# Performance work log

Measured on AMD Instinct MI355X. Metric: run time of the kernel, lower is better.

The kernel has to match this reference:

```python
import jax, jax.numpy as jnp
import numpy as np

SHORT = 2000
CUTVALS = [0, 2000, 12000, 40000, 100000]  # [0] + cutoffs + [n_classes]
OSZ = [10000, 28000, 60000]
HSZ = [384, 192, 96]
IN_F = 768
LN_EPS = 1e-5


def setup_inputs() -> dict:
    key = jax.random.key(0)
    ks = jax.random.split(key, 16)
    B, L = 256, 20
    inp = {
        "x": jax.random.normal(ks[0], (B, IN_F), jnp.float32),
        "head_W": jax.random.normal(ks[1], (SHORT + 3, IN_F), jnp.float32) / np.sqrt(IN_F),
        "target": jax.random.randint(ks[2], (B, L), 0, CUTVALS[-1], jnp.int64)
        if jax.config.jax_enable_x64 else jax.random.randint(ks[2], (B, L), 0, CUTVALS[-1], jnp.int32),
    }
    for i in range(3):
        inp[f"w1_{i}"] = jax.random.normal(ks[3 + 4 * i], (HSZ[i], IN_F), jnp.float32) / np.sqrt(IN_F)
        inp[f"g{i}"] = jnp.ones((HSZ[i],), jnp.float32)
        inp[f"b{i}"] = jnp.zeros((HSZ[i],), jnp.float32)
        inp[f"w2_{i}"] = jax.random.normal(ks[4 + 4 * i], (OSZ[i], HSZ[i]), jnp.float32) / np.sqrt(HSZ[i])
    return inp


def _bce_with_logits(logits, y):
    # matches torch BCEWithLogitsLoss(reduction='none')
    return jnp.maximum(logits, 0.0) - logits * y + jnp.log1p(jnp.exp(-jnp.abs(logits)))


def reference(x, head_W, w1_0, g0, b0, w2_0, w1_1, g1, b1, w2_1, w1_2, g2, b2, w2_2, target):
    W1, G, Bp, W2 = [w1_0, w1_1, w1_2], [g0, g1, g2], [b0, b1, b2], [w2_0, w2_1, w2_2]
    B = x.shape[0]
    rows = jnp.arange(B)[:, None]
    dt = x.dtype

    head_logits = x @ head_W.T  # [B, SHORT + n_clusters]

    # shortlist multi-hot (rows with no shortlist label stay all-zero, as in torch)
    m0 = target < SHORT
    onehot_short = jnp.zeros((B, SHORT), dt).at[rows, jnp.clip(target, 0, SHORT - 1)].max(m0.astype(dt))

    total_cluster = jnp.zeros((B,), dt)
    actives = []
    for i in range(3):
        low, high = CUTVALS[i + 1], CUTVALS[i + 2]
        osz = high - low
        m = (target >= low) & (target < high)  # [B, L]
        active = m.any(axis=1).astype(dt)      # [B]
        actives.append(active)
        # multi-hot targets for this cluster
        y = jnp.zeros((B, osz), dt).at[rows, jnp.clip(target - low, 0, osz - 1)].max(m.astype(dt))
        # tail projection: Linear -> LayerNorm -> ReLU -> Linear
        h = x @ W1[i].T
        mu = h.mean(-1, keepdims=True)
        var = ((h - mu) ** 2).mean(-1, keepdims=True)
        h = jax.nn.relu((h - mu) * jax.lax.rsqrt(var + LN_EPS) * G[i] + Bp[i])
        # p = sigmoid(cluster-root logit) * sigmoid(tail logits)
        root = jax.nn.sigmoid(head_logits[:, SHORT + i])[:, None]  # [B,1]
        p = root * jax.nn.sigmoid(h @ W2[i].T)                     # [B, osz]
        # torch BCELoss clamps log at -100
        bce = -(y * jnp.maximum(jnp.log(p), -100.0) + (1.0 - y) * jnp.maximum(jnp.log1p(-p), -100.0))
        total_cluster = total_cluster + active * bce.sum(axis=1)

    cluster_onehot = jnp.stack(actives, axis=1)  # [B, 3]
    head_y = jnp.concatenate([onehot_short, cluster_onehot], axis=1)
    head_loss = _bce_with_logits(head_logits, head_y)  # [B, SHORT+3]
    mult = (cluster_onehot == 0).astype(dt)
    head_loss = jnp.concatenate([head_loss[:, :SHORT], head_loss[:, SHORT:] * mult], axis=1)
    head_loss = head_loss.sum(axis=1)

    csz = jnp.asarray(OSZ, dt)
    num_loss = (mult + cluster_onehot * csz).sum(axis=1) + SHORT
    return ((head_loss + total_cluster) / num_loss).mean()
```

## Files before the change

### kernel.cpp

```cpp
#include <hip/hip_runtime.h>
#include <hip/hip_bf16.h>

#define INF 768
#define NSHORT 2000
#define NHEAD 2003

typedef __attribute__((ext_vector_type(8))) short  s16x8;
typedef __attribute__((ext_vector_type(4))) float  f32x4;
typedef __attribute__((ext_vector_type(8))) float  f32x8;

__device__ __forceinline__ float sigf(float z) { return 1.f / (1.f + __expf(-z)); }
__device__ __forceinline__ float softplusf(float z) {
    return fmaxf(z, 0.f) + __logf(1.f + __expf(-fabsf(z)));
}
__device__ __forceinline__ float qreduce16(float v) {
    v += __shfl_xor(v, 1); v += __shfl_xor(v, 2);
    v += __shfl_xor(v, 4); v += __shfl_xor(v, 8);
    return v;
}
__device__ __forceinline__ float wreduce64(float v) {
    v += __shfl_xor(v, 1);  v += __shfl_xor(v, 2);  v += __shfl_xor(v, 4);
    v += __shfl_xor(v, 8);  v += __shfl_xor(v, 16); v += __shfl_xor(v, 32);
    return v;
}
__device__ __forceinline__ short bfc(float x) {
    union { __hip_bfloat16 h; short s; } u; u.h = __float2bfloat16(x); return u.s;
}

template <int K32, int KC, int MODE, int AF32>
__device__ __forceinline__ void core_c(
    const void* __restrict__ Av, int kbase32,
    const float* __restrict__ W, int Kfull, int N, int stripe,
    short* __restrict__ lds,
    float* __restrict__ outH, int ldH,
    float* __restrict__ part, int pslot,
    const float* __restrict__ rootlogit, int ci)
{
    constexpr int NCH = K32 / KC;
    const int t = threadIdx.x;
    const int wave = t >> 6, lane = t & 63;
    const int quad = lane >> 4, l16 = lane & 15;
    const int rtb = wave * 4;

    const int sct = t >> 6, sl = t & 63;
    int scol = stripe * 64 + sct * 16 + (sl & 15);
    if (scol >= N) scol = N - 1;
    const float* wsrc = W + (size_t)scol * Kfull + kbase32 * 32 + (sl >> 4) * 8;

    size_t aoff[4];
#pragma unroll
    for (int rt = 0; rt < 4; rt++) {
        if (AF32)
            aoff[rt] = (size_t)((rtb + rt) * 16 + l16) * Kfull + kbase32 * 32 + quad * 8;
        else
            aoff[rt] = (size_t)(rtb + rt) * K32 * 512 + (size_t)lane * 8;
    }

#pragma unroll
    for (int s = 0; s < KC; s++) {
        const f32x8 v = *(const f32x8*)(wsrc + (size_t)s * 32);
        s16x8 o;
#pragma unroll
        for (int i = 0; i < 8; i++) o[i] = bfc(v[i]);
        *(s16x8*)(lds + (((size_t)s * 4 + sct) * 64 + sl) * 8) = o;
    }
    __syncthreads();

    f32x4 acc[4][4];
#pragma unroll
    for (int rt = 0; rt < 4; rt++)
#pragma unroll
        for (int ct = 0; ct < 4; ct++) acc[rt][ct] = (f32x4){0.f, 0.f, 0.f, 0.f};

#pragma unroll
    for (int c = 0; c < NCH; c++) {
        short* lbuf = lds + (size_t)(c & 1) * (KC * 2048);
        f32x8 nv[KC];
        if (c + 1 < NCH) {
#pragma unroll
            for (int s = 0; s < KC; s++)
                nv[s] = *(const f32x8*)(wsrc + ((size_t)((c + 1) * KC + s)) * 32);
        }
#pragma unroll
        for (int jj = 0; jj < KC; jj++) {
            const int jg = c * KC + jj;
            s16x8 af[4];
            if (AF32) {
#pragma unroll
                for (int rt = 0; rt < 4; rt++) {
                    const f32x8 v = *(const f32x8*)((const float*)Av + aoff[rt] + (size_t)jg * 32);
#pragma unroll
                    for (int i = 0; i < 8; i++) af[rt][i] = bfc(v[i]);
                }
            } else {
#pragma unroll
                for (int rt = 0; rt < 4; rt++)
                    af[rt] = *(const s16x8*)((const short*)Av + aoff[rt] + (size_t)jg * 512);
            }
#pragma unroll
            for (int ct = 0; ct < 4; ct++) {
                const s16x8 wf = *(const s16x8*)(lbuf + (((size_t)jj * 4 + ct) * 64 + lane) * 8);
#pragma unroll
                for (int rt = 0; rt < 4; rt++)
                    acc[rt][ct] = __builtin_amdgcn_mfma_f32_16x16x32_bf16(
                        af[rt], wf, acc[rt][ct], 0, 0, 0);
            }
        }
        if (c + 1 < NCH) {
            short* nbuf = lds + (size_t)((c + 1) & 1) * (KC * 2048);
#pragma unroll
            for (int s = 0; s < KC; s++) {
                s16x8 o;
#pragma unroll
                for (int i = 0; i < 8; i++) o[i] = bfc(nv[s][i]);
                *(s16x8*)(nbuf + (((size_t)s * 4 + sct) * 64 + sl) * 8) = o;
            }
            __syncthreads();
        }
    }

    const int col0 = stripe * 64;
    if (MODE == 0) {
#pragma unroll
        for (int rt = 0; rt < 4; rt++)
#pragma unroll
            for (int ct = 0; ct < 4; ct++) {
                const int col = col0 + ct * 16 + l16;
                if (col < N) {
#pragma unroll
                    for (int r = 0; r < 4; r++)
                        outH[(size_t)((rtb + rt) * 16 + quad * 4 + r) * ldH + col] =
                            acc[rt][ct][r];
                }
            }
    } else {
#pragma unroll
        for (int rt = 0; rt < 4; rt++) {
#pragma unroll
            for (int r = 0; r < 4; r++) {
                const int row = (rtb + rt) * 16 + quad * 4 + r;
                const float rv = sigf(rootlogit[row * 3 + ci]);
                float pd = 1.f, pn = 1.f;
#pragma unroll
                for (int ct = 0; ct < 4; ct++) {
                    const int col = col0 + ct * 16 + l16;
                    const float tv = fminf(__expf(-acc[rt][ct][r]), 1e6f);
                    const float d = (col < N) ? (1.f + tv) : 1.f;
                    const float n = (col < N) ? (1.f + tv - rv) : 1.f;
                    pd *= d; pn *= n;
                }
                float s = __logf(pd) - __logf(pn);
                s = qreduce16(s);
                if (l16 == 0) part[(size_t)pslot * 256 + row] = s;
            }
        }
    }
}

__global__ __launch_bounds__(256, 2) void k_mm1(
    const float* __restrict__ x, const float* __restrict__ headW,
    const float* __restrict__ w10, const float* __restrict__ w11,
    const float* __restrict__ w12,
    float* __restrict__ zbase,
    float* __restrict__ h0base,
    float* __restrict__ h1base,
    float* __restrict__ h2base,
    float* __restrict__ rootlogit)
{
    __shared__ __align__(16) short smem[8192];
    const int bx = blockIdx.x;
    if (bx < 128) {
        const int stripe = bx >> 2, kq = bx & 3;
        core_c<6, 2, 0, 1>(x, kq * 6, headW, INF, NHEAD, stripe, smem,
                           zbase + (size_t)kq * 256 * 2048, 2048,
                           nullptr, 0, nullptr, 0);
    } else if (bx < 172) {
        const int m = bx - 128;
        if (m < 24) {
            const int stripe = m >> 2, kq = m & 3;
            core_c<6, 2, 0, 1>(x, kq * 6, w10, INF, 384, stripe, smem,
                               h0base + (size_t)kq * 256 * 384, 384,
                               nullptr, 0, nullptr, 0);
        } else if (m < 36) {
            const int m2 = m - 24, stripe = m2 >> 2, kq = m2 & 3;
            core_c<6, 2, 0, 1>(x, kq * 6, w11, INF, 192, stripe, smem,
                               h1base + (size_t)kq * 256 * 192, 192,
                               nullptr, 0, nullptr, 0);
        } else {
            const int m2 = m - 36, stripe = m2 >> 2, kq = m2 & 3;
            core_c<6, 2, 0, 1>(x, kq * 6, w12, INF, 96, stripe, smem,
                               h2base + (size_t)kq * 256 * 96, 96,
                               nullptr, 0, nullptr, 0);
        }
    } else {
        const int row = bx - 172, wave = threadIdx.x >> 6, lane = threadIdx.x & 63;
        if (wave < 3) {
            const float* xr = x + row * INF;
            const float* wr = headW + (size_t)(NSHORT + wave) * INF;
            float s = 0.f;
            for (int k = lane; k < INF; k += 64) s += xr[k] * wr[k];
            s = wreduce64(s);
            if (lane == 0) rootlogit[row * 3 + wave] = s;
        }
    }
}

__global__ __launch_bounds__(256) void k_ln(const float* __restrict__ h0base,
                                            const float* __restrict__ h1base,
                                            const float* __restrict__ h2base,
                                            const float* g0, const float* g1, const float* g2,
                                            const float* b0, const float* b1, const float* b2,
                                            const float* __restrict__ zbase,
                                            __hip_bfloat16* f0, __hip_bfloat16* f1,
                                            __hip_bfloat16* f2,
                                            __hip_bfloat16* p0, __hip_bfloat16* p1,
                                            __hip_bfloat16* p2,
                                            float* __restrict__ phead,
                                            float* __restrict__ out) {
    const int bx = blockIdx.x;
    if (bx == 0 && threadIdx.x == 0) out[0] = 0.f;
    if (bx < 192) {
        const int task = bx * 4 + (threadIdx.x >> 6);
        const int ci = task >> 8, row = task & 255, lane = threadIdx.x & 63;
        const float *hb, *g, *bb; __hip_bfloat16 *fo, *po; int hsz, K32;
        if (ci == 0)      { hb = h0base; g = g0; bb = b0; fo = f0; po = p0; hsz = 384; K32 = 12; }
        else if (ci == 1) { hb = h1base; g = g1; bb = b1; fo = f1; po = p1; hsz = 192; K32 = 6; }
        else              { hb = h2base; g = g2; bb = b2; fo = f2; po = p2; hsz = 96;  K32 = 3; }
        const size_t qs = (size_t)256 * hsz;
        const float* hr = hb + (size_t)row * hsz;
        float s = 0.f, s2 = 0.f;
        for (int k = lane; k < hsz; k += 64) {
            const float v = hr[k] + hr[qs + k] + hr[2 * qs + k] + hr[3 * qs + k];
            s += v; s2 += v * v;
        }
        s = wreduce64(s); s2 = wreduce64(s2);
        const float mu = s / hsz;
        const float var = s2 / hsz - mu * mu;
        const float rsn = rsqrtf(var + 1e-5f);
        const int nch = hsz >> 3;
        if (lane < nch) {
            f32x8 v = *(const f32x8*)(hr + lane * 8);
            const f32x8 v1 = *(const f32x8*)(hr + qs + lane * 8);
            const f32x8 v2 = *(const f32x8*)(hr + 2 * qs + lane * 8);
            const f32x8 v3 = *(const f32x8*)(hr + 3 * qs + lane * 8);
            const f32x8 gg = *(const f32x8*)(g + lane * 8);
            const f32x8 bv = *(const f32x8*)(bb + lane * 8);
            s16x8 o;
#pragma unroll
            for (int i = 0; i < 8; i++) {
                const float hv = v[i] + v1[i] + v2[i] + v3[i];
                o[i] = bfc(fmaxf((hv - mu) * rsn * gg[i] + bv[i], 0.f));
            }
            *(s16x8*)((short*)fo + (size_t)row * hsz + lane * 8) = o;
            const size_t chunk = ((size_t)(row >> 4) * K32 + (lane >> 2)) * 64
                               + (lane & 3) * 16 + (row & 15);
            *(s16x8*)((short*)po + chunk * 8) = o;
        }
    } else {
        const int row = bx - 192, t = threadIdx.x;
        const int wave = t >> 6, lane = t & 63;
        float val = 0.f;
        if (t < 250) {
            const size_t base = (size_t)row * 2048 + t * 8;
            const f32x8 a = *(const f32x8*)(zbase + base);
            const f32x8 b = *(const f32x8*)(zbase + 524288 + base);
            const f32x8 c = *(const f32x8*)(zbase + 2 * 524288 + base);
            const f32x8 d = *(const f32x8*)(zbase + 3 * 524288 + base);
            float m = 0.f, P = 1.f;
#pragma unroll
            for (int i = 0; i < 8; i++) {
                const float z = a[i] + b[i] + c[i] + d[i];
                m += fmaxf(z, 0.f);
                P *= 1.f + __expf(-fabsf(z));
            }
            val = m + __logf(P);
        }
        val = wreduce64(val);
        __shared__ float red[4];
        if (lane == 0) red[wave] = val;
        __syncthreads();
        if (t == 0) phead[row] = red[0] + red[1] + red[2] + red[3];
    }
}

__global__ __launch_bounds__(256, 4) void k_bce(const __hip_bfloat16* p0,
                                                const __hip_bfloat16* p1,
                                                const __hip_bfloat16* p2,
                                                const float* __restrict__ w20,
                                                const float* __restrict__ w21,
                                                const float* __restrict__ w22,
                                                float* __restrict__ part,
                                                const float* __restrict__ rootlogit) {
    __shared__ __align__(16) short smem[8192];
    const int s = blockIdx.x;
    if (s < 157)
        core_c<12, 2, 2, 0>(p0, 0, w20, 384, 10000, s, smem,
                            nullptr, 0, part, s, rootlogit, 0);
    else if (s < 595)
        core_c<6, 2, 2, 0>(p1, 0, w21, 192, 28000, s - 157, smem,
                           nullptr, 0, part, s, rootlogit, 1);
    else
        core_c<3, 3, 2, 0>(p2, 0, w22, 96, 60000, s - 595, smem,
                           nullptr, 0, part, s, rootlogit, 2);
}

__global__ __launch_bounds__(256) void k_red(const float* __restrict__ part,
                                             const float* __restrict__ phead,
                                             const float* __restrict__ rootlogit,
                                             const int* __restrict__ target,
                                             const float* __restrict__ x,
                                             const float* __restrict__ headW,
                                             const __hip_bfloat16* f0,
                                             const __hip_bfloat16* f1,
                                             const __hip_bfloat16* f2,
                                             const float* w20, const float* w21, const float* w22,
                                             float* __restrict__ out) {
    const int row = blockIdx.x;
    const int t = threadIdx.x, wave = t >> 6, lane = t & 63;
    __shared__ float sx[INF];
    __shared__ __hip_bfloat16 shb[384 + 192 + 96];
    __shared__ int st[20];
    __shared__ float scorr[4];
    __shared__ float red[4][4];
    for (int i = t; i < INF; i += 256) sx[i] = x[row * INF + i];
    for (int i = t; i < 384; i += 256) shb[i] = f0[row * 384 + i];
    for (int i = t; i < 192; i += 256) shb[384 + i] = f1[row * 192 + i];
    for (int i = t; i < 96; i += 256)  shb[576 + i] = f2[row * 96 + i];
    if (t < 20) st[t] = target[row * 20 + t];
    if (t < 4) scorr[t] = 0.f;
    __syncthreads();
    for (int l = wave; l < 20; l += 4) {
        const int tg = st[l];
        bool dup = false;
        for (int m = 0; m < l; m++) dup |= (st[m] == tg);
        if (dup) continue;
        if (tg < NSHORT) {
            const float* wr = headW + (size_t)tg * INF;
            float z = 0.f;
            for (int k = lane; k < INF; k += 64) z += sx[k] * wr[k];
            z = wreduce64(z);
            if (lane == 0) atomicAdd(&scorr[3], -z);
        } else {
            int ci, low, hsz, hoff; const float* w2;
            if (tg < 12000)      { ci = 0; low = 2000;  hsz = 384; hoff = 0;   w2 = w20; }
            else if (tg < 40000) { ci = 1; low = 12000; hsz = 192; hoff = 384; w2 = w21; }
            else                 { ci = 2; low = 40000; hsz = 96;  hoff = 576; w2 = w22; }
            const float* wr = w2 + (size_t)(tg - low) * hsz;
            float z = 0.f;
            for (int k = lane; k < hsz; k += 64)
                z += __bfloat162float(shb[hoff + k]) * wr[k];
            z = wreduce64(z);
            if (lane == 0) {
                const float rvv = sigf(rootlogit[row * 3 + ci]);
                const float p = rvv * sigf(z);
                atomicAdd(&scorr[ci],
                          -fmaxf(__logf(p), -100.f) + fmaxf(__logf(1.f - p), -100.f));
            }
        }
    }
    float c0 = 0.f, c1 = 0.f, c2 = 0.f;
    for (int i = t; i < 1533; i += 256) {
        const float v = part[(size_t)i * 256 + row];
        if (i < 157) c0 += v; else if (i < 595) c1 += v; else c2 += v;
    }
    c0 = wreduce64(c0); c1 = wreduce64(c1); c2 = wreduce64(c2);
    if (lane == 0) { red[0][wave] = c0; red[1][wave] = c1; red[2][wave] = c2; }
    __syncthreads();
    if (t == 0) {
        float cc[3];
        for (int i = 0; i < 3; i++) cc[i] = red[i][0] + red[i][1] + red[i][2] + red[i][3];
        float hsum = phead[row] + scorr[3];
        bool act[3] = {false, false, false};
        for (int l = 0; l < 20; l++) {
            const int tg = target[row * 20 + l];
            if (tg >= 2000) {
                if (tg < 12000) act[0] = true;
                else if (tg < 40000) act[1] = true;
                else act[2] = true;
            }
        }
        float total = 0.f, num = 2000.f;
        const float csz[3] = {10000.f, 28000.f, 60000.f};
        for (int i = 0; i < 3; i++) {
            if (act[i]) { total += cc[i] + scorr[i]; num += csz[i]; }
            else        { hsum += softplusf(rootlogit[row * 3 + i]); num += 1.f; }
        }
        atomicAdd(out, (hsum + total) / num * (1.f / 256.f));
    }
}

extern "C" void kernel_launch(void* const* d_in, const int* in_sizes, int n_in,
                              void* d_out, int out_size, void* d_ws, size_t ws_size,
                              hipStream_t stream) {
    const float* x      = (const float*)d_in[0];
    const float* headW  = (const float*)d_in[1];
    const int*   target = (const int*)d_in[2];
    const float* w10 = (const float*)d_in[3];
    const float* g0  = (const float*)d_in[4];
    const float* b0  = (const float*)d_in[5];
    const float* w20 = (const float*)d_in[6];
    const float* w11 = (const float*)d_in[7];
    const float* g1  = (const float*)d_in[8];
    const float* b1  = (const float*)d_in[9];
    const float* w21 = (const float*)d_in[10];
    const float* w12 = (const float*)d_in[11];
    const float* g2  = (const float*)d_in[12];
    const float* b2  = (const float*)d_in[13];
    const float* w22 = (const float*)d_in[14];
    float* out = (float*)d_out;

    char* ws = (char*)d_ws;
    size_t off = 0;
    auto carve = [&](size_t bytes) -> void* {
        void* p = ws + off;
        off += (bytes + 255) & ~(size_t)255;
        return p;
    };
    float* zbase         = (float*)carve((size_t)4 * 256 * 2048 * 4);
    float* h0base        = (float*)carve((size_t)4 * 256 * 384 * 4);
    float* h1base        = (float*)carve((size_t)4 * 256 * 192 * 4);
    float* h2base        = (float*)carve((size_t)4 * 256 * 96 * 4);
    __hip_bfloat16* f0   = (__hip_bfloat16*)carve((size_t)256 * 384 * 2);
    __hip_bfloat16* f1   = (__hip_bfloat16*)carve((size_t)256 * 192 * 2);
    __hip_bfloat16* f2   = (__hip_bfloat16*)carve((size_t)256 * 96 * 2);
    __hip_bfloat16* p0   = (__hip_bfloat16*)carve((size_t)256 * 384 * 2);
    __hip_bfloat16* p1   = (__hip_bfloat16*)carve((size_t)256 * 192 * 2);
    __hip_bfloat16* p2   = (__hip_bfloat16*)carve((size_t)256 * 96 * 2);
    float* rootlogit     = (float*)carve((size_t)256 * 3 * 4);
    float* phead         = (float*)carve((size_t)256 * 4);
    float* part          = (float*)carve((size_t)1536 * 256 * 4);

    k_mm1<<<428, 256, 0, stream>>>(x, headW, w10, w11, w12,
                                   zbase, h0base, h1base, h2base, rootlogit);
    k_ln<<<448, 256, 0, stream>>>(h0base, h1base, h2base,
                                  g0, g1, g2, b0, b1, b2, zbase,
                                  f0, f1, f2, p0, p1, p2, phead, out);
    k_bce<<<1533, 256, 0, stream>>>(p0, p1, p2, w20, w21, w22, part, rootlogit);
    k_red<<<256, 256, 0, stream>>>(part, phead, rootlogit, target, x, headW,
                                   f0, f1, f2, w20, w21, w22, out);

    (void)in_sizes; (void)n_in; (void)out_size; (void)ws_size;
}
```

Baseline: 182.3 us.

## Fuse four kernels into one persistent kernel with grid-wide barriers

```diff
diff --git a/kernel.cpp b/kernel.cpp
--- a/kernel.cpp
+++ b/kernel.cpp
@@ -4,6 +4,7 @@
 #define INF 768
 #define NSHORT 2000
 #define NHEAD 2003
+#define GRID 768
 
 typedef __attribute__((ext_vector_type(8))) short  s16x8;
 typedef __attribute__((ext_vector_type(4))) float  f32x4;
@@ -25,6 +26,18 @@
 }
 __device__ __forceinline__ short bfc(float x) {
     union { __hip_bfloat16 h; short s; } u; u.h = __float2bfloat16(x); return u.s;
+}
+
+__device__ __forceinline__ void gsync(int* bar) {
+    __syncthreads();
+    if (threadIdx.x == 0) {
+        __threadfence();
+        atomicAdd(bar, 1);
+        while (__hip_atomic_load(bar, __ATOMIC_ACQUIRE, __HIP_MEMORY_SCOPE_AGENT) < GRID)
+            __builtin_amdgcn_s_sleep(4);
+        __threadfence();
+    }
+    __syncthreads();
 }
 
 template <int K32, int KC, int MODE, int AF32>
@@ -56,6 +69,8 @@
             aoff[rt] = (size_t)(rtb + rt) * K32 * 512 + (size_t)lane * 8;
     }
 
+    __syncthreads();
+
 #pragma unroll
     for (int s = 0; s < KC; s++) {
         const f32x8 v = *(const f32x8*)(wsrc + (size_t)s * 32);
@@ -108,6 +123,7 @@
         }
         if (c + 1 < NCH) {
             short* nbuf = lds + (size_t)((c + 1) & 1) * (KC * 2048);
+            __syncthreads();
 #pragma unroll
             for (int s = 0; s < KC; s++) {
                 s16x8 o;
@@ -157,75 +173,68 @@
     }
 }
 
-__global__ __launch_bounds__(256, 2) void k_mm1(
-    const float* __restrict__ x, const float* __restrict__ headW,
-    const float* __restrict__ w10, const float* __restrict__ w11,
-    const float* __restrict__ w12,
-    float* __restrict__ zbase,
-    float* __restrict__ h0base,
-    float* __restrict__ h1base,
-    float* __restrict__ h2base,
-    float* __restrict__ rootlogit)
-{
+struct Params {
+    const float *x, *headW, *w10, *w11, *w12, *w20, *w21, *w22;
+    const float *g0, *g1, *g2, *b0, *b1, *b2;
+    const int* target;
+    float *zbase, *h0base, *h1base, *h2base;
+    __hip_bfloat16 *f0, *f1, *f2, *p0, *p1, *p2;
+    float *rootlogit, *phead, *part;
+    int* bar;
+    float* out;
+};
+
+__global__ __launch_bounds__(256, 3) void k_fused(Params P) {
     __shared__ __align__(16) short smem[8192];
-    const int bx = blockIdx.x;
+    const int bx = blockIdx.x, t = threadIdx.x;
+    const int wave = t >> 6, lane = t & 63;
+
     if (bx < 128) {
         const int stripe = bx >> 2, kq = bx & 3;
-        core_c<6, 2, 0, 1>(x, kq * 6, headW, INF, NHEAD, stripe, smem,
-                           zbase + (size_t)kq * 256 * 2048, 2048,
+        core_c<6, 2, 0, 1>(P.x, kq * 6, P.headW, INF, NHEAD, stripe, smem,
+                           P.zbase + (size_t)kq * 256 * 2048, 2048,
                            nullptr, 0, nullptr, 0);
     } else if (bx < 172) {
         const int m = bx - 128;
         if (m < 24) {
             const int stripe = m >> 2, kq = m & 3;
-            core_c<6, 2, 0, 1>(x, kq * 6, w10, INF, 384, stripe, smem,
-                               h0base + (size_t)kq * 256 * 384, 384,
+            core_c<6, 2, 0, 1>(P.x, kq * 6, P.w10, INF, 384, stripe, smem,
+                               P.h0base + (size_t)kq * 256 * 384, 384,
                                nullptr, 0, nullptr, 0);
         } else if (m < 36) {
             const int m2 = m - 24, stripe = m2 >> 2, kq = m2 & 3;
-            core_c<6, 2, 0, 1>(x, kq * 6, w11, INF, 192, stripe, smem,
-                               h1base + (size_t)kq * 256 * 192, 192,
+            core_c<6, 2, 0, 1>(P.x, kq * 6, P.w11, INF, 192, stripe, smem,
+                               P.h1base + (size_t)kq * 256 * 192, 192,
                                nullptr, 0, nullptr, 0);
         } else {
             const int m2 = m - 36, stripe = m2 >> 2, kq = m2 & 3;
-            core_c<6, 2, 0, 1>(x, kq * 6, w12, INF, 96, stripe, smem,
-                               h2base + (size_t)kq * 256 * 96, 96,
+            core_c<6, 2, 0, 1>(P.x, kq * 6, P.w12, INF, 96, stripe, smem,
+                               P.h2base + (size_t)kq * 256 * 96, 96,
                                nullptr, 0, nullptr, 0);
         }
-    } else {
-        const int row = bx - 172, wave = threadIdx.x >> 6, lane = threadIdx.x & 63;
+    } else if (bx < 428) {
+        const int row = bx - 172;
         if (wave < 3) {
-            const float* xr = x + row * INF;
-            const float* wr = headW + (size_t)(NSHORT + wave) * INF;
+            const float* xr = P.x + row * INF;
+            const float* wr = P.headW + (size_t)(NSHORT + wave) * INF;
             float s = 0.f;
             for (int k = lane; k < INF; k += 64) s += xr[k] * wr[k];
             s = wreduce64(s);
-            if (lane == 0) rootlogit[row * 3 + wave] = s;
-        }
-    }
-}
-
-__global__ __launch_bounds__(256) void k_ln(const float* __restrict__ h0base,
-                                            const float* __restrict__ h1base,
-                                            const float* __restrict__ h2base,
-                                            const float* g0, const float* g1, const float* g2,
-                                            const float* b0, const float* b1, const float* b2,
-                                            const float* __restrict__ zbase,
-                                            __hip_bfloat16* f0, __hip_bfloat16* f1,
-                                            __hip_bfloat16* f2,
-                                            __hip_bfloat16* p0, __hip_bfloat16* p1,
-                                            __hip_bfloat16* p2,
-                                            float* __restrict__ phead,
-                                            float* __restrict__ out) {
-    const int bx = blockIdx.x;
-    if (bx == 0 && threadIdx.x == 0) out[0] = 0.f;
+            if (lane == 0) P.rootlogit[row * 3 + wave] = s;
+        }
+    } else if (bx == 700 && t == 0) {
+        P.out[0] = 0.f;
+    }
+
+    gsync(P.bar + 0);
+
     if (bx < 192) {
-        const int task = bx * 4 + (threadIdx.x >> 6);
-        const int ci = task >> 8, row = task & 255, lane = threadIdx.x & 63;
+        const int task = bx * 4 + wave;
+        const int ci = task >> 8, row = task & 255;
         const float *hb, *g, *bb; __hip_bfloat16 *fo, *po; int hsz, K32;
-        if (ci == 0)      { hb = h0base; g = g0; bb = b0; fo = f0; po = p0; hsz = 384; K32 = 12; }
-        else if (ci == 1) { hb = h1base; g = g1; bb = b1; fo = f1; po = p1; hsz = 192; K32 = 6; }
-        else              { hb = h2base; g = g2; bb = b2; fo = f2; po = p2; hsz = 96;  K32 = 3; }
+        if (ci == 0)      { hb = P.h0base; g = P.g0; bb = P.b0; fo = P.f0; po = P.p0; hsz = 384; K32 = 12; }
+        else if (ci == 1) { hb = P.h1base; g = P.g1; bb = P.b1; fo = P.f1; po = P.p1; hsz = 192; K32 = 6; }
+        else              { hb = P.h2base; g = P.g2; bb = P.b2; fo = P.f2; po = P.p2; hsz = 96;  K32 = 3; }
         const size_t qs = (size_t)256 * hsz;
         const float* hr = hb + (size_t)row * hsz;
         float s = 0.f, s2 = 0.f;
@@ -239,7 +248,7 @@
         const float rsn = rsqrtf(var + 1e-5f);
         const int nch = hsz >> 3;
         if (lane < nch) {
-            f32x8 v = *(const f32x8*)(hr + lane * 8);
+            const f32x8 v0 = *(const f32x8*)(hr + lane * 8);
             const f32x8 v1 = *(const f32x8*)(hr + qs + lane * 8);
             const f32x8 v2 = *(const f32x8*)(hr + 2 * qs + lane * 8);
             const f32x8 v3 = *(const f32x8*)(hr + 3 * qs + lane * 8);
@@ -248,7 +257,7 @@
             s16x8 o;
 #pragma unroll
             for (int i = 0; i < 8; i++) {
-                const float hv = v[i] + v1[i] + v2[i] + v3[i];
+                const float hv = v0[i] + v1[i] + v2[i] + v3[i];
                 o[i] = bfc(fmaxf((hv - mu) * rsn * gg[i] + bv[i], 0.f));
             }
             *(s16x8*)((short*)fo + (size_t)row * hsz + lane * 8) = o;
@@ -256,158 +265,143 @@
                                + (lane & 3) * 16 + (row & 15);
             *(s16x8*)((short*)po + chunk * 8) = o;
         }
-    } else {
-        const int row = bx - 192, t = threadIdx.x;
-        const int wave = t >> 6, lane = t & 63;
+    } else if (bx < 448) {
+        const int row = bx - 192;
         float val = 0.f;
         if (t < 250) {
             const size_t base = (size_t)row * 2048 + t * 8;
-            const f32x8 a = *(const f32x8*)(zbase + base);
-            const f32x8 b = *(const f32x8*)(zbase + 524288 + base);
-            const f32x8 c = *(const f32x8*)(zbase + 2 * 524288 + base);
-            const f32x8 d = *(const f32x8*)(zbase + 3 * 524288 + base);
-            float m = 0.f, P = 1.f;
+            const f32x8 a = *(const f32x8*)(P.zbase + base);
+            const f32x8 b = *(const f32x8*)(P.zbase + 524288 + base);
+            const f32x8 c = *(const f32x8*)(P.zbase + 2 * 524288 + base);
+            const f32x8 d = *(const f32x8*)(P.zbase + 3 * 524288 + base);
+            float m = 0.f, Pp = 1.f;
 #pragma unroll
             for (int i = 0; i < 8; i++) {
                 const float z = a[i] + b[i] + c[i] + d[i];
                 m += fmaxf(z, 0.f);
-                P *= 1.f + __expf(-fabsf(z));
-            }
-            val = m + __logf(P);
+                Pp *= 1.f + __expf(-fabsf(z));
+            }
+            val = m + __logf(Pp);
         }
         val = wreduce64(val);
-        __shared__ float red[4];
-        if (lane == 0) red[wave] = val;
+        float* red4 = (float*)smem;
+        if (lane == 0) red4[wave] = val;
         __syncthreads();
-        if (t == 0) phead[row] = red[0] + red[1] + red[2] + red[3];
-    }
-}
-
-__global__ __launch_bounds__(256, 4) void k_bce(const __hip_bfloat16* p0,
-                                                const __hip_bfloat16* p1,
-                                                const __hip_bfloat16* p2,
-                                                const float* __restrict__ w20,
-                                                const float* __restrict__ w21,
-                                                const float* __restrict__ w22,
-                                                float* __restrict__ part,
-                                                const float* __restrict__ rootlogit) {
-    __shared__ __align__(16) short smem[8192];
-    const int s = blockIdx.x;
-    if (s < 157)
-        core_c<12, 2, 2, 0>(p0, 0, w20, 384, 10000, s, smem,
-                            nullptr, 0, part, s, rootlogit, 0);
-    else if (s < 595)
-        core_c<6, 2, 2, 0>(p1, 0, w21, 192, 28000, s - 157, smem,
-                           nullptr, 0, part, s, rootlogit, 1);
-    else
-        core_c<3, 3, 2, 0>(p2, 0, w22, 96, 60000, s - 595, smem,
-                           nullptr, 0, part, s, rootlogit, 2);
-}
-
-__global__ __launch_bounds__(256) void k_red(const float* __restrict__ part,
-                                             const float* __restrict__ phead,
-                                             const float* __restrict__ rootlogit,
-                                             const int* __restrict__ target,
-                                             const float* __restrict__ x,
-                                             const float* __restrict__ headW,
-                                             const __hip_bfloat16* f0,
-                                             const __hip_bfloat16* f1,
-                                             const __hip_bfloat16* f2,
-                                             const float* w20, const float* w21, const float* w22,
-                                             float* __restrict__ out) {
-    const int row = blockIdx.x;
-    const int t = threadIdx.x, wave = t >> 6, lane = t & 63;
-    __shared__ float sx[INF];
-    __shared__ __hip_bfloat16 shb[384 + 192 + 96];
-    __shared__ int st[20];
-    __shared__ float scorr[4];
-    __shared__ float red[4][4];
-    for (int i = t; i < INF; i += 256) sx[i] = x[row * INF + i];
-    for (int i = t; i < 384; i += 256) shb[i] = f0[row * 384 + i];
-    for (int i = t; i < 192; i += 256) shb[384 + i] = f1[row * 192 + i];
-    for (int i = t; i < 96; i += 256)  shb[576 + i] = f2[row * 96 + i];
-    if (t < 20) st[t] = target[row * 20 + t];
-    if (t < 4) scorr[t] = 0.f;
-    __syncthreads();
-    for (int l = wave; l < 20; l += 4) {
-        const int tg = st[l];
-        bool dup = false;
-        for (int m = 0; m < l; m++) dup |= (st[m] == tg);
-        if (dup) continue;
-        if (tg < NSHORT) {
-            const float* wr = headW + (size_t)tg * INF;
-            float z = 0.f;
-            for (int k = lane; k < INF; k += 64) z += sx[k] * wr[k];
-            z = wreduce64(z);
-            if (lane == 0) atomicAdd(&scorr[3], -z);
-        } else {
-            int ci, low, hsz, hoff; const float* w2;
-            if (tg < 12000)      { ci = 0; low = 2000;  hsz = 384; hoff = 0;   w2 = w20; }
-            else if (tg < 40000) { ci = 1; low = 12000; hsz = 192; hoff = 384; w2 = w21; }
-            else                 { ci = 2; low = 40000; hsz = 96;  hoff = 576; w2 = w22; }
-            const float* wr = w2 + (size_t)(tg - low) * hsz;
-            float z = 0.f;
-            for (int k = lane; k < hsz; k += 64)
-                z += __bfloat162float(shb[hoff + k]) * wr[k];
-            z = wreduce64(z);
-            if (lane == 0) {
-                const float rvv = sigf(rootlogit[row * 3 + ci]);
-                const float p = rvv * sigf(z);
-                atomicAdd(&scorr[ci],
-                          -fmaxf(__logf(p), -100.f) + fmaxf(__logf(1.f - p), -100.f));
-            }
-        }
-    }
-    float c0 = 0.f, c1 = 0.f, c2 = 0.f;
-    for (int i = t; i < 1533; i += 256) {
-        const float v = part[(size_t)i * 256 + row];
-        if (i < 157) c0 += v; else if (i < 595) c1 += v; else c2 += v;
-    }
-    c0 = wreduce64(c0); c1 = wreduce64(c1); c2 = wreduce64(c2);
-    if (lane == 0) { red[0][wave] = c0; red[1][wave] = c1; red[2][wave] = c2; }
-    __syncthreads();
-    if (t == 0) {
-        float cc[3];
-        for (int i = 0; i < 3; i++) cc[i] = red[i][0] + red[i][1] + red[i][2] + red[i][3];
-        float hsum = phead[row] + scorr[3];
-        bool act[3] = {false, false, false};
-        for (int l = 0; l < 20; l++) {
-            const int tg = target[row * 20 + l];
-            if (tg >= 2000) {
-                if (tg < 12000) act[0] = true;
-                else if (tg < 40000) act[1] = true;
-                else act[2] = true;
-            }
-        }
-        float total = 0.f, num = 2000.f;
-        const float csz[3] = {10000.f, 28000.f, 60000.f};
-        for (int i = 0; i < 3; i++) {
-            if (act[i]) { total += cc[i] + scorr[i]; num += csz[i]; }
-            else        { hsum += softplusf(rootlogit[row * 3 + i]); num += 1.f; }
-        }
-        atomicAdd(out, (hsum + total) / num * (1.f / 256.f));
+        if (t == 0) P.phead[row] = red4[0] + red4[1] + red4[2] + red4[3];
+    }
+
+    gsync(P.bar + 1);
+
+    for (int s = bx; s < 1533; s += GRID) {
+        if (s < 157)
+            core_c<12, 2, 2, 0>(P.p0, 0, P.w20, 384, 10000, s, smem,
+                                nullptr, 0, P.part, s, P.rootlogit, 0);
+        else if (s < 595)
+            core_c<6, 2, 2, 0>(P.p1, 0, P.w21, 192, 28000, s - 157, smem,
+                               nullptr, 0, P.part, s, P.rootlogit, 1);
+        else
+            core_c<3, 3, 2, 0>(P.p2, 0, P.w22, 96, 60000, s - 595, smem,
+                               nullptr, 0, P.part, s, P.rootlogit, 2);
+    }
+
+    gsync(P.bar + 2);
+
+    if (bx < 256) {
+        const int row = bx;
+        char* sm = (char*)smem;
+        float* sx = (float*)sm;
+        __hip_bfloat16* shb = (__hip_bfloat16*)(sm + 3072);
+        int* st = (int*)(sm + 4480);
+        float* scorr = (float*)(sm + 4608);
+        float (*red)[4] = (float(*)[4])(sm + 4672);
+        for (int i = t; i < INF; i += 256) sx[i] = P.x[row * INF + i];
+        for (int i = t; i < 384; i += 256) shb[i] = P.f0[row * 384 + i];
+        for (int i = t; i < 192; i += 256) shb[384 + i] = P.f1[row * 192 + i];
+        for (int i = t; i < 96; i += 256)  shb[576 + i] = P.f2[row * 96 + i];
+        if (t < 20) st[t] = P.target[row * 20 + t];
+        if (t < 4) scorr[t] = 0.f;
+        __syncthreads();
+        for (int l = wave; l < 20; l += 4) {
+            const int tg = st[l];
+            bool dup = false;
+            for (int m = 0; m < l; m++) dup |= (st[m] == tg);
+            if (dup) continue;
+            if (tg < NSHORT) {
+                const float* wr = P.headW + (size_t)tg * INF;
+                float z = 0.f;
+                for (int k = lane; k < INF; k += 64) z += sx[k] * wr[k];
+                z = wreduce64(z);
+                if (lane == 0) atomicAdd(&scorr[3], -z);
+            } else {
+                int ci, low, hsz, hoff; const float* w2;
+                if (tg < 12000)      { ci = 0; low = 2000;  hsz = 384; hoff = 0;   w2 = P.w20; }
+                else if (tg < 40000) { ci = 1; low = 12000; hsz = 192; hoff = 384; w2 = P.w21; }
+                else                 { ci = 2; low = 40000; hsz = 96;  hoff = 576; w2 = P.w22; }
+                const float* wr = w2 + (size_t)(tg - low) * hsz;
+                float z = 0.f;
+                for (int k = lane; k < hsz; k += 64)
+                    z += __bfloat162float(shb[hoff + k]) * wr[k];
+                z = wreduce64(z);
+                if (lane == 0) {
+                    const float rvv = sigf(P.rootlogit[row * 3 + ci]);
+                    const float p = rvv * sigf(z);
+                    atomicAdd(&scorr[ci],
+                              -fmaxf(__logf(p), -100.f) + fmaxf(__logf(1.f - p), -100.f));
+                }
+            }
+        }
+        float c0 = 0.f, c1 = 0.f, c2 = 0.f;
+        for (int i = t; i < 1533; i += 256) {
+            const float v = P.part[(size_t)i * 256 + row];
+            if (i < 157) c0 += v; else if (i < 595) c1 += v; else c2 += v;
+        }
+        c0 = wreduce64(c0); c1 = wreduce64(c1); c2 = wreduce64(c2);
+        if (lane == 0) { red[0][wave] = c0; red[1][wave] = c1; red[2][wave] = c2; }
+        __syncthreads();
+        if (t == 0) {
+            float cc[3];
+            for (int i = 0; i < 3; i++) cc[i] = red[i][0] + red[i][1] + red[i][2] + red[i][3];
+            float hsum = P.phead[row] + scorr[3];
+            bool act[3] = {false, false, false};
+            for (int l = 0; l < 20; l++) {
+                const int tg = P.target[row * 20 + l];
+                if (tg >= 2000) {
+                    if (tg < 12000) act[0] = true;
+                    else if (tg < 40000) act[1] = true;
+                    else act[2] = true;
+                }
+            }
+            float total = 0.f, num = 2000.f;
+            const float csz[3] = {10000.f, 28000.f, 60000.f};
+            for (int i = 0; i < 3; i++) {
+                if (act[i]) { total += cc[i] + scorr[i]; num += csz[i]; }
+                else        { hsum += softplusf(P.rootlogit[row * 3 + i]); num += 1.f; }
+            }
+            atomicAdd(P.out, (hsum + total) / num * (1.f / 256.f));
+        }
     }
 }
 
 extern "C" void kernel_launch(void* const* d_in, const int* in_sizes, int n_in,
                               void* d_out, int out_size, void* d_ws, size_t ws_size,
                               hipStream_t stream) {
-    const float* x      = (const float*)d_in[0];
-    const float* headW  = (const float*)d_in[1];
-    const int*   target = (const int*)d_in[2];
-    const float* w10 = (const float*)d_in[3];
-    const float* g0  = (const float*)d_in[4];
-    const float* b0  = (const float*)d_in[5];
-    const float* w20 = (const float*)d_in[6];
-    const float* w11 = (const float*)d_in[7];
-    const float* g1  = (const float*)d_in[8];
-    const float* b1  = (const float*)d_in[9];
-    const float* w21 = (const float*)d_in[10];
-    const float* w12 = (const float*)d_in[11];
-    const float* g2  = (const float*)d_in[12];
-    const float* b2  = (const float*)d_in[13];
-    const float* w22 = (const float*)d_in[14];
-    float* out = (float*)d_out;
+    Params P;
+    P.x      = (const float*)d_in[0];
+    P.headW  = (const float*)d_in[1];
+    P.target = (const int*)d_in[2];
+    P.w10 = (const float*)d_in[3];
+    P.g0  = (const float*)d_in[4];
+    P.b0  = (const float*)d_in[5];
+    P.w20 = (const float*)d_in[6];
+    P.w11 = (const float*)d_in[7];
+    P.g1  = (const float*)d_in[8];
+    P.b1  = (const float*)d_in[9];
+    P.w21 = (const float*)d_in[10];
+    P.w12 = (const float*)d_in[11];
+    P.g2  = (const float*)d_in[12];
+    P.b2  = (const float*)d_in[13];
+    P.w22 = (const float*)d_in[14];
+    P.out = (float*)d_out;
 
     char* ws = (char*)d_ws;
     size_t off = 0;
@@ -416,28 +410,23 @@
         off += (bytes + 255) & ~(size_t)255;
         return p;
     };
-    float* zbase         = (float*)carve((size_t)4 * 256 * 2048 * 4);
-    float* h0base        = (float*)carve((size_t)4 * 256 * 384 * 4);
-    float* h1base        = (float*)carve((size_t)4 * 256 * 192 * 4);
-    float* h2base        = (float*)carve((size_t)4 * 256 * 96 * 4);
-    __hip_bfloat16* f0   = (__hip_bfloat16*)carve((size_t)256 * 384 * 2);
-    __hip_bfloat16* f1   = (__hip_bfloat16*)carve((size_t)256 * 192 * 2);
-    __hip_bfloat16* f2   = (__hip_bfloat16*)carve((size_t)256 * 96 * 2);
-    __hip_bfloat16* p0   = (__hip_bfloat16*)carve((size_t)256 * 384 * 2);
-    __hip_bfloat16* p1   = (__hip_bfloat16*)carve((size_t)256 * 192 * 2);
-    __hip_bfloat16* p2   = (__hip_bfloat16*)carve((size_t)256 * 96 * 2);
-    float* rootlogit     = (float*)carve((size_t)256 * 3 * 4);
-    float* phead         = (float*)carve((size_t)256 * 4);
-    float* part          = (float*)carve((size_t)1536 * 256 * 4);
-
-    k_mm1<<<428, 256, 0, stream>>>(x, headW, w10, w11, w12,
-                                   zbase, h0base, h1base, h2base, rootlogit);
-    k_ln<<<448, 256, 0, stream>>>(h0base, h1base, h2base,
-                                  g0, g1, g2, b0, b1, b2, zbase,
-                                  f0, f1, f2, p0, p1, p2, phead, out);
-    k_bce<<<1533, 256, 0, stream>>>(p0, p1, p2, w20, w21, w22, part, rootlogit);
-    k_red<<<256, 256, 0, stream>>>(part, phead, rootlogit, target, x, headW,
-                                   f0, f1, f2, w20, w21, w22, out);
+    P.zbase     = (float*)carve((size_t)4 * 256 * 2048 * 4);
+    P.h0base    = (float*)carve((size_t)4 * 256 * 384 * 4);
+    P.h1base    = (float*)carve((size_t)4 * 256 * 192 * 4);
+    P.h2base    = (float*)carve((size_t)4 * 256 * 96 * 4);
+    P.f0        = (__hip_bfloat16*)carve((size_t)256 * 384 * 2);
+    P.f1        = (__hip_bfloat16*)carve((size_t)256 * 192 * 2);
+    P.f2        = (__hip_bfloat16*)carve((size_t)256 * 96 * 2);
+    P.p0        = (__hip_bfloat16*)carve((size_t)256 * 384 * 2);
+    P.p1        = (__hip_bfloat16*)carve((size_t)256 * 192 * 2);
+    P.p2        = (__hip_bfloat16*)carve((size_t)256 * 96 * 2);
+    P.rootlogit = (float*)carve((size_t)256 * 3 * 4);
+    P.phead     = (float*)carve((size_t)256 * 4);
+    P.part      = (float*)carve((size_t)1536 * 256 * 4);
+    P.bar       = (int*)carve(256);
+
+    hipMemsetAsync(P.bar, 0, 3 * sizeof(int), stream);
+    k_fused<<<GRID, 256, 0, stream>>>(P);
 
     (void)in_sizes; (void)n_in; (void)out_size; (void)ws_size;
 }
```

After: 630.6 us. 3.46x slower.

## Drop split-K partials, fuse head BCE into GEMM epilogue, add one-shot tail weight loader

Applied to the files above, without the earlier changes.

```diff
diff --git a/kernel.cpp b/kernel.cpp
--- a/kernel.cpp
+++ b/kernel.cpp
@@ -108,6 +108,7 @@
         }
         if (c + 1 < NCH) {
             short* nbuf = lds + (size_t)((c + 1) & 1) * (KC * 2048);
+            __syncthreads();
 #pragma unroll
             for (int s = 0; s < KC; s++) {
                 s16x8 o;
@@ -133,6 +134,27 @@
                             acc[rt][ct][r];
                 }
             }
+    } else if (MODE == 1) {
+#pragma unroll
+        for (int rt = 0; rt < 4; rt++) {
+#pragma unroll
+            for (int r = 0; r < 4; r++) {
+                const int row = (rtb + rt) * 16 + quad * 4 + r;
+                float m = 0.f, Pp = 1.f;
+#pragma unroll
+                for (int ct = 0; ct < 4; ct++) {
+                    const int col = col0 + ct * 16 + l16;
+                    if (col < NSHORT) {
+                        const float z = acc[rt][ct][r];
+                        m += fmaxf(z, 0.f);
+                        Pp *= 1.f + __expf(-fabsf(z));
+                    }
+                }
+                float s = m + __logf(Pp);
+                s = qreduce16(s);
+                if (l16 == 0) part[(size_t)pslot * 256 + row] = s;
+            }
+        }
     } else {
 #pragma unroll
         for (int rt = 0; rt < 4; rt++) {
@@ -157,43 +179,123 @@
     }
 }
 
-__global__ __launch_bounds__(256, 2) void k_mm1(
+template <int K32>
+__device__ __forceinline__ void core_b(
+    const __hip_bfloat16* __restrict__ Ap,
+    const float* __restrict__ W, int N, int stripe,
+    short* __restrict__ lds,
+    float* __restrict__ part, int pslot,
+    const float* __restrict__ rootlogit, int ci)
+{
+    const int t = threadIdx.x;
+    const int wave = t >> 6, lane = t & 63;
+    const int quad = lane >> 4, l16 = lane & 15;
+    const int rtb = wave * 4;
+    const int Kfull = K32 * 32;
+
+    const int sct = t >> 6, sl = t & 63;
+    int scol = stripe * 64 + sct * 16 + (sl & 15);
+    if (scol >= N) scol = N - 1;
+    const float* wsrc = W + (size_t)scol * Kfull + (sl >> 4) * 8;
+    short* wdst = lds + ((size_t)sct * 64 + sl) * 8;
+
+    constexpr int G = (K32 <= 6) ? K32 : 6;
+    constexpr int NG = K32 / G;
+    f32x8 buf[G];
+#pragma unroll
+    for (int s = 0; s < G; s++) buf[s] = *(const f32x8*)(wsrc + (size_t)s * 32);
+#pragma unroll
+    for (int gg = 0; gg < NG; gg++) {
+        f32x8 nbuf[G];
+        if (gg + 1 < NG) {
+#pragma unroll
+            for (int s = 0; s < G; s++)
+                nbuf[s] = *(const f32x8*)(wsrc + (size_t)((gg + 1) * G + s) * 32);
+        }
+#pragma unroll
+        for (int s = 0; s < G; s++) {
+            s16x8 o;
+#pragma unroll
+            for (int i = 0; i < 8; i++) o[i] = bfc(buf[s][i]);
+            *(s16x8*)(wdst + (size_t)(gg * G + s) * 2048) = o;
+        }
+        if (gg + 1 < NG) {
+#pragma unroll
+            for (int s = 0; s < G; s++) buf[s] = nbuf[s];
+        }
+    }
+    __syncthreads();
+
+    const short* abase = (const short*)Ap + (size_t)lane * 8;
+    f32x4 acc[4][4];
+#pragma unroll
+    for (int rt = 0; rt < 4; rt++)
+#pragma unroll
+        for (int ct = 0; ct < 4; ct++) acc[rt][ct] = (f32x4){0.f, 0.f, 0.f, 0.f};
+
+#pragma unroll
+    for (int j = 0; j < K32; j++) {
+        s16x8 af[4];
+#pragma unroll
+        for (int rt = 0; rt < 4; rt++)
+            af[rt] = *(const s16x8*)(abase + (size_t)((rtb + rt) * K32 + j) * 512);
+#pragma unroll
+        for (int ct = 0; ct < 4; ct++) {
+            const s16x8 wf = *(const s16x8*)(lds + (((size_t)j * 4 + ct) * 64 + lane) * 8);
+#pragma unroll
+            for (int rt = 0; rt < 4; rt++)
+                acc[rt][ct] = __builtin_amdgcn_mfma_f32_16x16x32_bf16(
+                    af[rt], wf, acc[rt][ct], 0, 0, 0);
+        }
+    }
+
+    const int col0 = stripe * 64;
+#pragma unroll
+    for (int rt = 0; rt < 4; rt++) {
+#pragma unroll
+        for (int r = 0; r < 4; r++) {
+            const int row = (rtb + rt) * 16 + quad * 4 + r;
+            const float rv = sigf(rootlogit[row * 3 + ci]);
+            float pd = 1.f, pn = 1.f;
+#pragma unroll
+            for (int ct = 0; ct < 4; ct++) {
+                const int col = col0 + ct * 16 + l16;
+                const float tv = fminf(__expf(-acc[rt][ct][r]), 1e6f);
+                const float d = (col < N) ? (1.f + tv) : 1.f;
+                const float n = (col < N) ? (1.f + tv - rv) : 1.f;
+                pd *= d; pn *= n;
+            }
+            float s = __logf(pd) - __logf(pn);
+            s = qreduce16(s);
+            if (l16 == 0) part[(size_t)pslot * 256 + row] = s;
+        }
+    }
+}
+
+__global__ __launch_bounds__(256) void k_mm1(
     const float* __restrict__ x, const float* __restrict__ headW,
     const float* __restrict__ w10, const float* __restrict__ w11,
     const float* __restrict__ w12,
-    float* __restrict__ zbase,
-    float* __restrict__ h0base,
-    float* __restrict__ h1base,
-    float* __restrict__ h2base,
+    float* __restrict__ phead,
+    float* h0, float* h1, float* h2,
     float* __restrict__ rootlogit)
 {
-    __shared__ __align__(16) short smem[8192];
+    __shared__ __align__(16) short smem[16384];
     const int bx = blockIdx.x;
-    if (bx < 128) {
-        const int stripe = bx >> 2, kq = bx & 3;
-        core_c<6, 2, 0, 1>(x, kq * 6, headW, INF, NHEAD, stripe, smem,
-                           zbase + (size_t)kq * 256 * 2048, 2048,
-                           nullptr, 0, nullptr, 0);
-    } else if (bx < 172) {
-        const int m = bx - 128;
-        if (m < 24) {
-            const int stripe = m >> 2, kq = m & 3;
-            core_c<6, 2, 0, 1>(x, kq * 6, w10, INF, 384, stripe, smem,
-                               h0base + (size_t)kq * 256 * 384, 384,
-                               nullptr, 0, nullptr, 0);
-        } else if (m < 36) {
-            const int m2 = m - 24, stripe = m2 >> 2, kq = m2 & 3;
-            core_c<6, 2, 0, 1>(x, kq * 6, w11, INF, 192, stripe, smem,
-                               h1base + (size_t)kq * 256 * 192, 192,
-                               nullptr, 0, nullptr, 0);
-        } else {
-            const int m2 = m - 36, stripe = m2 >> 2, kq = m2 & 3;
-            core_c<6, 2, 0, 1>(x, kq * 6, w12, INF, 96, stripe, smem,
-                               h2base + (size_t)kq * 256 * 96, 96,
-                               nullptr, 0, nullptr, 0);
-        }
+    if (bx < 32) {
+        core_c<24, 4, 1, 1>(x, 0, headW, INF, NHEAD, bx, smem,
+                            nullptr, 0, phead, bx, nullptr, 0);
+    } else if (bx < 38) {
+        core_c<24, 4, 0, 1>(x, 0, w10, INF, 384, bx - 32, smem,
+                            h0, 384, nullptr, 0, nullptr, 0);
+    } else if (bx < 41) {
+        core_c<24, 4, 0, 1>(x, 0, w11, INF, 192, bx - 38, smem,
+                            h1, 192, nullptr, 0, nullptr, 0);
+    } else if (bx < 43) {
+        core_c<24, 4, 0, 1>(x, 0, w12, INF, 96, bx - 41, smem,
+                            h2, 96, nullptr, 0, nullptr, 0);
     } else {
-        const int row = bx - 172, wave = threadIdx.x >> 6, lane = threadIdx.x & 63;
+        const int row = bx - 43, wave = threadIdx.x >> 6, lane = threadIdx.x & 63;
         if (wave < 3) {
             const float* xr = x + row * INF;
             const float* wr = headW + (size_t)(NSHORT + wave) * INF;
@@ -205,103 +307,60 @@
     }
 }
 
-__global__ __launch_bounds__(256) void k_ln(const float* __restrict__ h0base,
-                                            const float* __restrict__ h1base,
-                                            const float* __restrict__ h2base,
+__global__ __launch_bounds__(256) void k_ln(const float* h0, const float* h1, const float* h2,
                                             const float* g0, const float* g1, const float* g2,
                                             const float* b0, const float* b1, const float* b2,
-                                            const float* __restrict__ zbase,
                                             __hip_bfloat16* f0, __hip_bfloat16* f1,
                                             __hip_bfloat16* f2,
                                             __hip_bfloat16* p0, __hip_bfloat16* p1,
                                             __hip_bfloat16* p2,
-                                            float* __restrict__ phead,
                                             float* __restrict__ out) {
-    const int bx = blockIdx.x;
-    if (bx == 0 && threadIdx.x == 0) out[0] = 0.f;
-    if (bx < 192) {
-        const int task = bx * 4 + (threadIdx.x >> 6);
-        const int ci = task >> 8, row = task & 255, lane = threadIdx.x & 63;
-        const float *hb, *g, *bb; __hip_bfloat16 *fo, *po; int hsz, K32;
-        if (ci == 0)      { hb = h0base; g = g0; bb = b0; fo = f0; po = p0; hsz = 384; K32 = 12; }
-        else if (ci == 1) { hb = h1base; g = g1; bb = b1; fo = f1; po = p1; hsz = 192; K32 = 6; }
-        else              { hb = h2base; g = g2; bb = b2; fo = f2; po = p2; hsz = 96;  K32 = 3; }
-        const size_t qs = (size_t)256 * hsz;
-        const float* hr = hb + (size_t)row * hsz;
-        float s = 0.f, s2 = 0.f;
-        for (int k = lane; k < hsz; k += 64) {
-            const float v = hr[k] + hr[qs + k] + hr[2 * qs + k] + hr[3 * qs + k];
-            s += v; s2 += v * v;
-        }
-        s = wreduce64(s); s2 = wreduce64(s2);
-        const float mu = s / hsz;
-        const float var = s2 / hsz - mu * mu;
-        const float rsn = rsqrtf(var + 1e-5f);
-        const int nch = hsz >> 3;
-        if (lane < nch) {
-            f32x8 v = *(const f32x8*)(hr + lane * 8);
-            const f32x8 v1 = *(const f32x8*)(hr + qs + lane * 8);
-            const f32x8 v2 = *(const f32x8*)(hr + 2 * qs + lane * 8);
-            const f32x8 v3 = *(const f32x8*)(hr + 3 * qs + lane * 8);
-            const f32x8 gg = *(const f32x8*)(g + lane * 8);
-            const f32x8 bv = *(const f32x8*)(bb + lane * 8);
-            s16x8 o;
-#pragma unroll
-            for (int i = 0; i < 8; i++) {
-                const float hv = v[i] + v1[i] + v2[i] + v3[i];
-                o[i] = bfc(fmaxf((hv - mu) * rsn * gg[i] + bv[i], 0.f));
-            }
-            *(s16x8*)((short*)fo + (size_t)row * hsz + lane * 8) = o;
-            const size_t chunk = ((size_t)(row >> 4) * K32 + (lane >> 2)) * 64
-                               + (lane & 3) * 16 + (row & 15);
-            *(s16x8*)((short*)po + chunk * 8) = o;
-        }
-    } else {
-        const int row = bx - 192, t = threadIdx.x;
-        const int wave = t >> 6, lane = t & 63;
-        float val = 0.f;
-        if (t < 250) {
-            const size_t base = (size_t)row * 2048 + t * 8;
-            const f32x8 a = *(const f32x8*)(zbase + base);
-            const f32x8 b = *(const f32x8*)(zbase + 524288 + base);
-            const f32x8 c = *(const f32x8*)(zbase + 2 * 524288 + base);
-            const f32x8 d = *(const f32x8*)(zbase + 3 * 524288 + base);
-            float m = 0.f, P = 1.f;
-#pragma unroll
-            for (int i = 0; i < 8; i++) {
-                const float z = a[i] + b[i] + c[i] + d[i];
-                m += fmaxf(z, 0.f);
-                P *= 1.f + __expf(-fabsf(z));
-            }
-            val = m + __logf(P);
-        }
-        val = wreduce64(val);
-        __shared__ float red[4];
-        if (lane == 0) red[wave] = val;
-        __syncthreads();
-        if (t == 0) phead[row] = red[0] + red[1] + red[2] + red[3];
-    }
-}
-
-__global__ __launch_bounds__(256, 4) void k_bce(const __hip_bfloat16* p0,
-                                                const __hip_bfloat16* p1,
-                                                const __hip_bfloat16* p2,
-                                                const float* __restrict__ w20,
-                                                const float* __restrict__ w21,
-                                                const float* __restrict__ w22,
-                                                float* __restrict__ part,
-                                                const float* __restrict__ rootlogit) {
-    __shared__ __align__(16) short smem[8192];
+    if (blockIdx.x == 0 && threadIdx.x == 0) out[0] = 0.f;
+    const int task = blockIdx.x * 4 + (threadIdx.x >> 6);
+    const int ci = task >> 8, row = task & 255, lane = threadIdx.x & 63;
+    const float *h, *g, *bb; __hip_bfloat16 *fo, *po; int hsz, K32;
+    if (ci == 0)      { h = h0; g = g0; bb = b0; fo = f0; po = p0; hsz = 384; K32 = 12; }
+    else if (ci == 1) { h = h1; g = g1; bb = b1; fo = f1; po = p1; hsz = 192; K32 = 6; }
+    else              { h = h2; g = g2; bb = b2; fo = f2; po = p2; hsz = 96;  K32 = 3; }
+    const float* hr = h + (size_t)row * hsz;
+    float s = 0.f, s2 = 0.f;
+    for (int k = lane; k < hsz; k += 64) { const float v = hr[k]; s += v; s2 += v * v; }
+    s = wreduce64(s); s2 = wreduce64(s2);
+    const float mu = s / hsz;
+    const float var = s2 / hsz - mu * mu;
+    const float rsn = rsqrtf(var + 1e-5f);
+    const int nch = hsz >> 3;
+    if (lane < nch) {
+        const f32x8 v = *(const f32x8*)(hr + lane * 8);
+        const f32x8 gg = *(const f32x8*)(g + lane * 8);
+        const f32x8 bv = *(const f32x8*)(bb + lane * 8);
+        s16x8 o;
+#pragma unroll
+        for (int i = 0; i < 8; i++)
+            o[i] = bfc(fmaxf((v[i] - mu) * rsn * gg[i] + bv[i], 0.f));
+        *(s16x8*)((short*)fo + (size_t)row * hsz + lane * 8) = o;
+        const size_t chunk = ((size_t)(row >> 4) * K32 + (lane >> 2)) * 64
+                           + (lane & 3) * 16 + (row & 15);
+        *(s16x8*)((short*)po + chunk * 8) = o;
+    }
+}
+
+__global__ __launch_bounds__(256) void k_bce(const __hip_bfloat16* p0,
+                                             const __hip_bfloat16* p1,
+                                             const __hip_bfloat16* p2,
+                                             const float* __restrict__ w20,
+                                             const float* __restrict__ w21,
+                                             const float* __restrict__ w22,
+                                             float* __restrict__ part,
+                                             const float* __restrict__ rootlogit) {
+    __shared__ __align__(16) short smem[24576];
     const int s = blockIdx.x;
     if (s < 157)
-        core_c<12, 2, 2, 0>(p0, 0, w20, 384, 10000, s, smem,
-                            nullptr, 0, part, s, rootlogit, 0);
+        core_b<12>(p0, w20, 10000, s, smem, part, s, rootlogit, 0);
     else if (s < 595)
-        core_c<6, 2, 2, 0>(p1, 0, w21, 192, 28000, s - 157, smem,
-                           nullptr, 0, part, s, rootlogit, 1);
+        core_b<6>(p1, w21, 28000, s - 157, smem, part, s, rootlogit, 1);
     else
-        core_c<3, 3, 2, 0>(p2, 0, w22, 96, 60000, s - 595, smem,
-                           nullptr, 0, part, s, rootlogit, 2);
+        core_b<3>(p2, w22, 60000, s - 595, smem, part, s, rootlogit, 2);
 }
 
 __global__ __launch_bounds__(256) void k_red(const float* __restrict__ part,
@@ -358,18 +417,19 @@
             }
         }
     }
-    float c0 = 0.f, c1 = 0.f, c2 = 0.f;
+    float c0 = 0.f, c1 = 0.f, c2 = 0.f, hs = 0.f;
     for (int i = t; i < 1533; i += 256) {
         const float v = part[(size_t)i * 256 + row];
         if (i < 157) c0 += v; else if (i < 595) c1 += v; else c2 += v;
     }
-    c0 = wreduce64(c0); c1 = wreduce64(c1); c2 = wreduce64(c2);
-    if (lane == 0) { red[0][wave] = c0; red[1][wave] = c1; red[2][wave] = c2; }
+    if (t < 32) hs = phead[(size_t)t * 256 + row];
+    c0 = wreduce64(c0); c1 = wreduce64(c1); c2 = wreduce64(c2); hs = wreduce64(hs);
+    if (lane == 0) { red[0][wave] = c0; red[1][wave] = c1; red[2][wave] = c2; red[3][wave] = hs; }
     __syncthreads();
     if (t == 0) {
         float cc[3];
         for (int i = 0; i < 3; i++) cc[i] = red[i][0] + red[i][1] + red[i][2] + red[i][3];
-        float hsum = phead[row] + scorr[3];
+        float hsum = red[3][0] + red[3][1] + red[3][2] + red[3][3] + scorr[3];
         bool act[3] = {false, false, false};
         for (int l = 0; l < 20; l++) {
             const int tg = target[row * 20 + l];
@@ -416,10 +476,9 @@
         off += (bytes + 255) & ~(size_t)255;
         return p;
     };
-    float* zbase         = (float*)carve((size_t)4 * 256 * 2048 * 4);
-    float* h0base        = (float*)carve((size_t)4 * 256 * 384 * 4);
-    float* h1base        = (float*)carve((size_t)4 * 256 * 192 * 4);
-    float* h2base        = (float*)carve((size_t)4 * 256 * 96 * 4);
+    float* h0            = (float*)carve((size_t)256 * 384 * 4);
+    float* h1            = (float*)carve((size_t)256 * 192 * 4);
+    float* h2            = (float*)carve((size_t)256 * 96 * 4);
     __hip_bfloat16* f0   = (__hip_bfloat16*)carve((size_t)256 * 384 * 2);
     __hip_bfloat16* f1   = (__hip_bfloat16*)carve((size_t)256 * 192 * 2);
     __hip_bfloat16* f2   = (__hip_bfloat16*)carve((size_t)256 * 96 * 2);
@@ -427,14 +486,13 @@
     __hip_bfloat16* p1   = (__hip_bfloat16*)carve((size_t)256 * 192 * 2);
     __hip_bfloat16* p2   = (__hip_bfloat16*)carve((size_t)256 * 96 * 2);
     float* rootlogit     = (float*)carve((size_t)256 * 3 * 4);
-    float* phead         = (float*)carve((size_t)256 * 4);
+    float* phead         = (float*)carve((size_t)32 * 256 * 4);
     float* part          = (float*)carve((size_t)1536 * 256 * 4);
 
-    k_mm1<<<428, 256, 0, stream>>>(x, headW, w10, w11, w12,
-                                   zbase, h0base, h1base, h2base, rootlogit);
-    k_ln<<<448, 256, 0, stream>>>(h0base, h1base, h2base,
-                                  g0, g1, g2, b0, b1, b2, zbase,
-                                  f0, f1, f2, p0, p1, p2, phead, out);
+    k_mm1<<<299, 256, 0, stream>>>(x, headW, w10, w11, w12,
+                                   phead, h0, h1, h2, rootlogit);
+    k_ln<<<192, 256, 0, stream>>>(h0, h1, h2, g0, g1, g2, b0, b1, b2,
+                                  f0, f1, f2, p0, p1, p2, out);
     k_bce<<<1533, 256, 0, stream>>>(p0, p1, p2, w20, w21, w22, part, rootlogit);
     k_red<<<256, 256, 0, stream>>>(part, phead, rootlogit, target, x, headW,
                                    f0, f1, f2, w20, w21, w22, out);
```

Result: slower. 219.9 us (+20.6%).
